# Performance work log

Measured on AMD Instinct MI355X. Metric: run time of the kernel, lower is better.

The kernel has to match this reference:

```python
import jax, jax.numpy as jnp
import numpy as np

N = 30000; E = 480000; B = 60
IN = 200; ID = 128; H = 128
NEXP = 4; TOPK = 2; TEMP = 1.5
HEADS = 4; DH = H // HEADS


def _ln(x, g, b):
    mu = jnp.mean(x, -1, keepdims=True)
    var = jnp.var(x, -1, keepdims=True)
    return (x - mu) / jnp.sqrt(var + 1e-5) * g + b


def _seg_sum(d, i, n):
    return jax.ops.segment_sum(d, i, num_segments=n)


def setup_inputs():
    key = jax.random.key(0)
    kit = iter(jax.random.split(key, 80))
    def w(*s):
        return jax.random.normal(next(kit), s, jnp.float32) * 0.05
    inp = {}
    inp['x'] = jax.random.normal(next(kit), (N, IN), jnp.float32)
    inp['node_identity'] = jax.random.normal(next(kit), (N, ID), jnp.float32)
    inp['edge_index'] = jax.random.randint(next(kit), (2, E), 0, N)
    inp['batch'] = jnp.sort(jax.random.randint(next(kit), (N,), 0, B))
    inp.update(fe_W=w(IN, H), fe_b=jnp.zeros(H), fe_g=jnp.ones(H), fe_be=jnp.zeros(H))
    inp.update(ie_W=w(ID, H), ie_b=jnp.zeros(H), ie_g=jnp.ones(H), ie_be=jnp.zeros(H))
    inp.update(fuse_W=w(2 * H, H), fuse_b=jnp.zeros(H), fuse_g=jnp.ones(H), fuse_be=jnp.zeros(H))
    inp.update(router_W=w(2 * H, NEXP))
    inp.update(mlp_W1=w(H, H), mlp_b1=jnp.zeros(H), mlp_W2=w(H, H), mlp_b2=jnp.zeros(H))
    inp.update(cheb_W=w(2, 2, H, H), cheb_b=jnp.zeros((2, H)))
    inp.update(gt_Wq=w(2, H, H), gt_bq=jnp.zeros((2, H)), gt_Wk=w(2, H, H), gt_bk=jnp.zeros((2, H)),
               gt_Wv=w(2, H, H), gt_bv=jnp.zeros((2, H)), gt_Ws=w(2, H, H), gt_bs=jnp.zeros((2, H)))
    inp.update(gcn_W=w(2, H, H), gcn_b=jnp.zeros((2, H)))
    inp.update(pn_g=jnp.ones((NEXP, H)), pn_b=jnp.zeros((NEXP, H)), expert_scales=jnp.ones(NEXP))
    inp.update(h1_W=w(H, H), h1_b=jnp.zeros(H), h1_g=jnp.ones(H), h1_be=jnp.zeros(H))
    inp.update(h2_W=w(H, H // 2), h2_b=jnp.zeros(H // 2), h2_g=jnp.ones(H // 2), h2_be=jnp.zeros(H // 2))
    inp.update(h3_W=w(H // 2, 2), h3_b=jnp.zeros(2), logit_bias=jnp.zeros(2))
    return inp


def _forward(x, node_identity, edge_index, batch, fe_W, fe_b, fe_g, fe_be, ie_W, ie_b, ie_g, ie_be,
             fuse_W, fuse_b, fuse_g, fuse_be, router_W, mlp_W1, mlp_b1, mlp_W2, mlp_b2, cheb_W, cheb_b,
             gt_Wq, gt_bq, gt_Wk, gt_bk, gt_Wv, gt_bv, gt_Ws, gt_bs, gcn_W, gcn_b, pn_g, pn_b,
             expert_scales, h1_W, h1_b, h1_g, h1_be, h2_W, h2_b, h2_g, h2_be, h3_W, h3_b, logit_bias):
    relu = jax.nn.relu
    src, dst = edge_index[0], edge_index[1]
    # encoders + fuse
    h_x = relu(_ln(x @ fe_W + fe_b, fe_g, fe_be))
    h_id = relu(_ln(node_identity @ ie_W + ie_b, ie_g, ie_be))
    h_router = jnp.concatenate([h_x, h_id], -1)
    h = relu(_ln(h_router @ fuse_W + fuse_b, fuse_g, fuse_be))
    # noisy top-k router (eval: no noise, no dropout)
    node_logits = h_router @ router_W
    probs = jax.nn.softmax(node_logits / TEMP, -1)
    vals, idx = jax.lax.top_k(probs, TOPK)
    wts = vals / jnp.clip(jnp.sum(vals, -1, keepdims=True), 1e-9)
    gates = jnp.zeros_like(probs).at[jnp.arange(N)[:, None], idx].set(wts)  # [N, 4]
    # degree / normalization terms
    ones_e = jnp.ones(E, jnp.float32)
    deg = _seg_sum(ones_e, dst, N)
    dinv = jnp.where(deg > 0, jax.lax.rsqrt(jnp.maximum(deg, 1.0)), 0.0)
    dinvl = jax.lax.rsqrt(deg + 1.0)  # with self loops (GCN)
    enorm = dinv[src] * dinv[dst]
    enorml = dinvl[src] * dinvl[dst]
    def aprop(xx, en, di_self=None):
        out = _seg_sum(xx[src] * en[:, None], dst, N)
        if di_self is not None:
            out = out + xx * di_self[:, None]
        return out
    # Expert 0: MLP (2 layers)
    e0 = relu(h @ mlp_W1 + mlp_b1) @ mlp_W2 + mlp_b2
    # Expert 1: ChebNet K=2 (lambda_max=2 -> L_hat = -A_norm), 2 layers
    z = h
    for l in range(2):
        tx1 = -aprop(z, enorm)
        z = z @ cheb_W[l, 0] + tx1 @ cheb_W[l, 1] + cheb_b[l]
        if l == 0:
            z = relu(z)
    e1 = z
    # Expert 2: Graph Transformer, 2 layers, heads=4, root-weight skip
    z = h
    for l in range(2):
        q = (z @ gt_Wq[l] + gt_bq[l]).reshape(N, HEADS, DH)
        k = (z @ gt_Wk[l] + gt_bk[l]).reshape(N, HEADS, DH)
        v = (z @ gt_Wv[l] + gt_bv[l]).reshape(N, HEADS, DH)
        logits = jnp.sum(q[dst] * k[src], -1) * (1.0 / DH ** 0.5)  # [E, heads]
        m = jax.ops.segment_max(logits, dst, num_segments=N)
        m = jnp.where(jnp.isfinite(m), m, 0.0)
        p = jnp.exp(logits - m[dst])
        denom = jnp.clip(_seg_sum(p, dst, N), 1e-9)
        attn = p / denom[dst]
        agg = _seg_sum(attn[:, :, None] * v[src], dst, N).reshape(N, H)
        z = agg + z @ gt_Ws[l] + gt_bs[l]
        if l == 0:
            z = relu(z)
    e2 = z
    # Expert 3: GCN, 2 layers, self loops
    z = h
    for l in range(2):
        zw = z @ gcn_W[l]
        z = aprop(zw, enorml, dinvl * dinvl) + gcn_b[l]
        if l == 0:
            z = relu(z)
    e3 = z
    # per-expert post-norm, scale, gated combine + residual
    eo = jnp.stack([e0, e1, e2, e3], 0)  # [4, N, H]
    eo = _ln(eo, pn_g[:, None, :], pn_b[:, None, :]) * expert_scales[:, None, None]
    out = h + jnp.einsum('ne,enh->nh', gates, eo)
    # mean-pool readout per graph
    counts = jnp.clip(_seg_sum(jnp.ones(N, jnp.float32), batch, B), 1.0)
    pooled = _seg_sum(out, batch, B) / counts[:, None]
    # classification head
    zc = relu(_ln(pooled @ h1_W + h1_b, h1_g, h1_be))
    zc = relu(_ln(zc @ h2_W + h2_b, h2_g, h2_be))
    return zc @ h3_W + h3_b + logit_bias


def reference(x, node_identity, edge_index, batch, fe_W, fe_b, fe_g, fe_be, ie_W, ie_b, ie_g, ie_be,
              fuse_W, fuse_b, fuse_g, fuse_be, router_W, mlp_W1, mlp_b1, mlp_W2, mlp_b2, cheb_W, cheb_b,
              gt_Wq, gt_bq, gt_Wk, gt_bk, gt_Wv, gt_bv, gt_Ws, gt_bs, gcn_W, gcn_b, pn_g, pn_b,
              expert_scales, h1_W, h1_b, h1_g, h1_be, h2_W, h2_b, h2_g, h2_be, h3_W, h3_b, logit_bias):
    return _forward(x, node_identity, edge_index, batch, fe_W, fe_b, fe_g, fe_be, ie_W, ie_b, ie_g, ie_be,
                    fuse_W, fuse_b, fuse_g, fuse_be, router_W, mlp_W1, mlp_b1, mlp_W2, mlp_b2, cheb_W, cheb_b,
                    gt_Wq, gt_bq, gt_Wk, gt_bk, gt_Wv, gt_bv, gt_Ws, gt_bs, gcn_W, gcn_b, pn_g, pn_b,
                    expert_scales, h1_W, h1_b, h1_g, h1_be, h2_W, h2_b, h2_g, h2_be, h3_W, h3_b, logit_bias)
```

## Files before the change

### kernel.cpp

```cpp
#include <hip/hip_runtime.h>

#define PCH   32
#define NWT   19
#define SCH   2048

typedef unsigned short ushort_t;
typedef __attribute__((ext_vector_type(8))) short bf16x8;
typedef __attribute__((ext_vector_type(4))) float f32x4;

__device__ __forceinline__ float bf2f(unsigned int v) {
    return __uint_as_float(v << 16);
}
__device__ __forceinline__ unsigned int f2bu(float f) {
    unsigned int u = __float_as_uint(f);
    return (u + 0x7fffu + ((u >> 16) & 1u)) >> 16;
}
__device__ __forceinline__ void unpack8(uint4 u, float* f) {
    f[0] = bf2f(u.x & 0xffff); f[1] = bf2f(u.x >> 16);
    f[2] = bf2f(u.y & 0xffff); f[3] = bf2f(u.y >> 16);
    f[4] = bf2f(u.z & 0xffff); f[5] = bf2f(u.z >> 16);
    f[6] = bf2f(u.w & 0xffff); f[7] = bf2f(u.w >> 16);
}
__device__ __forceinline__ uint4 pack8(const float* f) {
    uint4 p;
// ... 182 lines not shown
    const int row_base = m0 + 16 * wv + q * 4;
#pragma unroll
    for (int t = 0; t < 8; t++) {
        float bb = c.bias[t * 16 + l16];
#pragma unroll
        for (int r = 0; r < 4; r++) acc[t][r] += bb;
    }
    float mean[4], inv[4];
#pragma unroll
    for (int r = 0; r < 4; r++) {
        float s = 0.f, sq = 0.f;
#pragma unroll
        for (int t = 0; t < 8; t++) { float v = acc[t][r]; s += v; sq = fmaf(v, v, sq); }
#pragma unroll
        for (int off = 1; off <= 8; off <<= 1) { s += __shfl_xor(s, off); sq += __shfl_xor(sq, off); }
        mean[r] = s * (1.f / 128.f);
        float var = sq * (1.f / 128.f) - mean[r] * mean[r];
        inv[r] = rsqrtf(var + 1e-5f);
    }
    float rl0[4] = {0, 0, 0, 0}, rl1[4] = {0, 0, 0, 0};
    float rl2[4] = {0, 0, 0, 0}, rl3[4] = {0, 0, 0, 0};
#pragma unroll
    for (int t = 0; t < 8; t++) {
        int col = t * 16 + l16;
        float gg = c.g[col], b2 = c.be[col];
        float4 rw = *(const float4*)(c.rW + col * 4);
#pragma unroll
        for (int r = 0; r < 4; r++) {
            float y = fmaxf(fmaf((acc[t][r] - mean[r]) * inv[r], gg, b2), 0.f);
            rl0[r] = fmaf(y, rw.x, rl0[r]);
            rl1[r] = fmaf(y, rw.y, rl1[r]);
            rl2[r] = fmaf(y, rw.z, rl2[r]);
            rl3[r] = fmaf(y, rw.w, rl3[r]);
            float other = __shfl_xor(y, 1);
            int row = row_base + r;
            if (!(l16 & 1) && row < M) {
                unsigned int pk = f2bu(y) | (f2bu(other) << 16);
                *(unsigned int*)(c.Cb + (size_t)row * 256 + col) = pk;
            }
        }
    }
#pragma unroll
    for (int r = 0; r < 4; r++) {
#pragma unroll
        for (int off = 1; off <= 8; off <<= 1) {
            rl0[r] += __shfl_xor(rl0[r], off);
            rl1[r] += __shfl_xor(rl1[r], off);
            rl2[r] += __shfl_xor(rl2[r], off);
            rl3[r] += __shfl_xor(rl3[r], off);
        }
        int row = row_base + r;
        if (l16 == 0 && row < M)
            *(float4*)(c.logits + (size_t)row * 4) = make_float4(rl0[r], rl1[r], rl2[r], rl3[r]);
    }
}

__global__ __launch_bounds__(256)
void scan3_enc_kernel(int* __restrict__ rowptr, const int* __restrict__ bsum,
                      const int* __restrict__ degi,
                      float* __restrict__ dinv, float* __restrict__ dinvl, int N,
                      EncCfg c0, EncCfg c1)
{
    __shared__ ushort_t As[64][40];
    __shared__ ushort_t Bs[128][40];
    int bx = blockIdx.x;
    int ns3 = (N + 255) >> 8;
    int gG = (N + 63) >> 6;
    if (bx < ns3) {
        int i = bx * 256 + threadIdx.x;
        if (i == 0) rowptr[0] = 0;
        if (i < N) {
            rowptr[i + 1] += bsum[i / SCH];
            float deg = (float)degi[i];
            dinv[i] = (deg > 0.f) ? rsqrtf(fmaxf(deg, 1.f)) : 0.f;
            dinvl[i] = rsqrtf(deg + 1.f);
        }
        return;
    }
    int b2 = bx - ns3;
    if (b2 < gG) gemm_f32_ln_dev(As, Bs, c0, b2, N);
    else gemm_f32_ln_dev(As, Bs, c1, b2 - gG, N);
}

__global__ void csr_topk_kernel(const int* __restrict__ src, const int* __restrict__ dst,
                                const int* __restrict__ rowptr, int* __restrict__ cursor,
                                int* __restrict__ csr,
                                const float* __restrict__ dinv, const float* __restrict__ dinvl,
                                float* __restrict__ ecA, float* __restrict__ ecB, int E,
                                const float* __restrict__ la, const float* __restrict__ lb,
                                float* __restrict__ gates, int N)
{
    int bx = blockIdx.x;
    int nc = (E + 255) >> 8;
    if (bx < nc) {
        int e = bx * 256 + threadIdx.x;
        if (e >= E) return;
        int d = dst[e];
        int s = src[e];
        int pos = atomicAdd(&cursor[d], 1);
        int o = rowptr[d] + pos;
        csr[o] = s;
        ecA[o] = dinv[d] * dinv[s];
        ecB[o] = dinvl[d] * dinvl[s];
        return;
    }
    int n = (bx - nc) * 256 + threadIdx.x;
    if (n >= N) return;
    float4 a = *(const float4*)(la + (size_t)n * 4);
    float4 b = *(const float4*)(lb + (size_t)n * 4);
    float l[4] = {(a.x + b.x) * (1.f / 1.5f), (a.y + b.y) * (1.f / 1.5f),
                  (a.z + b.z) * (1.f / 1.5f), (a.w + b.w) * (1.f / 1.5f)};
    float mx = fmaxf(fmaxf(l[0], l[1]), fmaxf(l[2], l[3]));
    float e4[4], ssum = 0.f;
#pragma unroll
    for (int i = 0; i < 4; i++) { e4[i] = expf(l[i] - mx); ssum += e4[i]; }
    float p[4];
#pragma unroll
    for (int i = 0; i < 4; i++) p[i] = e4[i] / ssum;
    int i0 = 0;
    for (int i = 1; i < 4; i++) if (p[i] > p[i0]) i0 = i;
    int i1 = -1;
    for (int i = 0; i < 4; i++) {
        if (i == i0) continue;
        if (i1 < 0 || p[i] > p[i1]) i1 = i;
    }
    float wsum = fmaxf(p[i0] + p[i1], 1e-9f);
    float gg[4] = {0.f, 0.f, 0.f, 0.f};
    gg[i0] = p[i0] / wsum;
    gg[i1] = p[i1] / wsum;
    *(float4*)(gates + (size_t)n * 4) = make_float4(gg[0], gg[1], gg[2], gg[3]);
}

__global__ __launch_bounds__(256)
void gemm_ln256_kernel(const ushort_t* __restrict__ A,
                       const ushort_t* __restrict__ Wt,
                       ushort_t* __restrict__ Cb, int M,
                       const float* __restrict__ bias,
                       const float* __restrict__ g, const float* __restrict__ be)
{
    const int K = 256;
    __shared__ ushort_t As[64][40];
    __shared__ ushort_t Bs[128][40];
    const int tid = threadIdx.x;
    const int m0 = blockIdx.x * 64;
    const int lane = tid & 63;
    const int wv = tid >> 6;
    const int q = lane >> 4;
    const int l16 = lane & 15;
    const int sar = tid >> 2;
    const int sak = (tid & 3) << 3;
    const int sbn = tid >> 1;
    const int sbk = (tid & 1) << 4;
    const bool arow_ok = (m0 + sar) < M;
    const ushort_t* Arow = A + (size_t)(m0 + sar) * K;
    const ushort_t* Wrow = Wt + (size_t)sbn * K;

    f32x4 acc[8];
#pragma unroll
    for (int t = 0; t < 8; t++) acc[t] = (f32x4){0.f, 0.f, 0.f, 0.f};

#pragma unroll
    for (int k0 = 0; k0 < K; k0 += 32) {
        uint4 apk = arow_ok ? *(const uint4*)(Arow + k0 + sak) : make_uint4(0, 0, 0, 0);
        uint4 b0 = *(const uint4*)(Wrow + k0 + sbk);
        uint4 b1 = *(const uint4*)(Wrow + k0 + sbk + 8);
        __syncthreads();
        *(uint4*)&As[sar][sak] = apk;
        *(uint4*)&Bs[sbn][sbk] = b0;
        *(uint4*)&Bs[sbn][sbk + 8] = b1;
        __syncthreads();
        bf16x8 af = *(const bf16x8*)&As[16 * wv + l16][q * 8];
#pragma unroll
        for (int t = 0; t < 8; t++) {
            bf16x8 bf = *(const bf16x8*)&Bs[t * 16 + l16][q * 8];
            acc[t] = __builtin_amdgcn_mfma_f32_16x16x32_bf16(af, bf, acc[t], 0, 0, 0);
        }
    }
    const int row_base = m0 + 16 * wv + q * 4;
#pragma unroll
    for (int t = 0; t < 8; t++) {
        float bb = bias[t * 16 + l16];
#pragma unroll
        for (int r = 0; r < 4; r++) acc[t][r] += bb;
    }
    float mean[4], inv[4];
#pragma unroll
    for (int r = 0; r < 4; r++) {
        float s = 0.f, sq = 0.f;
#pragma unroll
        for (int t = 0; t < 8; t++) { float v = acc[t][r]; s += v; sq = fmaf(v, v, sq); }
#pragma unroll
        for (int off = 1; off <= 8; off <<= 1) { s += __shfl_xor(s, off); sq += __shfl_xor(sq, off); }
        mean[r] = s * (1.f / 128.f);
        float var = sq * (1.f / 128.f) - mean[r] * mean[r];
        inv[r] = rsqrtf(var + 1e-5f);
    }
#pragma unroll
    for (int t = 0; t < 8; t++) {
        int col = t * 16 + l16;
        float gg = g[col], b2 = be[col];
#pragma unroll
        for (int r = 0; r < 4; r++) {
            float y = fmaxf(fmaf((acc[t][r] - mean[r]) * inv[r], gg, b2), 0.f);
            float other = __shfl_xor(y, 1);
            int row = row_base + r;
            if (!(l16 & 1) && row < M) {
                unsigned int pk = f2bu(y) | (f2bu(other) << 16);
                *(unsigned int*)(Cb + (size_t)row * 128 + col) = pk;
            }
        }
    }
}

template <int K>
__device__ __forceinline__ void gemm_bf_dev(ushort_t (*As)[40], ushort_t (*Bs)[40],
                                            const ushort_t* __restrict__ A,
                                            const ushort_t* __restrict__ Wt,
                                            ushort_t* __restrict__ Cb, int M,
                                            const float* __restrict__ bias, int relu, int bx)
{
    const int tid = threadIdx.x;
    const int m0 = bx * 64;
    const int lane = tid & 63;
    const int wv = tid >> 6;
    const int q = lane >> 4;
    const int l16 = lane & 15;
    const int sar = tid >> 2;
    const int sak = (tid & 3) << 3;
    const int sbn = tid >> 1;
    const int sbk = (tid & 1) << 4;
    const bool arow_ok = (m0 + sar) < M;
    const ushort_t* Arow = A + (size_t)(m0 + sar) * K;
    const ushort_t* Wrow = Wt + (size_t)sbn * K;

    f32x4 acc[8];
#pragma unroll
    for (int t = 0; t < 8; t++) acc[t] = (f32x4){0.f, 0.f, 0.f, 0.f};

#pragma unroll
    for (int k0 = 0; k0 < K; k0 += 32) {
        uint4 apk = arow_ok ? *(const uint4*)(Arow + k0 + sak) : make_uint4(0, 0, 0, 0);
        uint4 b0 = *(const uint4*)(Wrow + k0 + sbk);
        uint4 b1 = *(const uint4*)(Wrow + k0 + sbk + 8);
        __syncthreads();
        *(uint4*)&As[sar][sak] = apk;
        *(uint4*)&Bs[sbn][sbk] = b0;
        *(uint4*)&Bs[sbn][sbk + 8] = b1;
        __syncthreads();
        bf16x8 af = *(const bf16x8*)&As[16 * wv + l16][q * 8];
#pragma unroll
        for (int t = 0; t < 8; t++) {
            bf16x8 bf = *(const bf16x8*)&Bs[t * 16 + l16][q * 8];
            acc[t] = __builtin_amdgcn_mfma_f32_16x16x32_bf16(af, bf, acc[t], 0, 0, 0);
        }
    }
#pragma unroll
    for (int t = 0; t < 8; t++) {
        int col = t * 16 + l16;
        float bb = bias ? bias[col] : 0.f;
#pragma unroll
        for (int r = 0; r < 4; r++) {
            int row = m0 + 16 * wv + q * 4 + r;
            float val = acc[t][r] + bb;
            if (relu) val = fmaxf(val, 0.f);
            float other = __shfl_xor(val, 1);
            if (!(lane & 1) && row < M) {
                unsigned int pk = f2bu(val) | (f2bu(other) << 16);
                *(unsigned int*)(Cb + (size_t)row * 128 + col) = pk;
            }
        }
    }
}

__device__ __forceinline__ void gemm_dual_dev(ushort_t (*As)[40], ushort_t (*Bs)[40],
                                              const ushort_t* __restrict__ A1,
                                              const ushort_t* __restrict__ Wt1,
                                              const ushort_t* __restrict__ A2,
                                              const ushort_t* __restrict__ Wt2,
                                              ushort_t* __restrict__ Cb, int M,
                                              const float* __restrict__ bias, int relu, int bx)
{
    const int K = 128;
    const int tid = threadIdx.x;
    const int m0 = bx * 64;
    const int lane = tid & 63;
    const int wv = tid >> 6;
    const int q = lane >> 4;
    const int l16 = lane & 15;
    const int sar = tid >> 2;
    const int sak = (tid & 3) << 3;
    const int sbn = tid >> 1;
    const int sbk = (tid & 1) << 4;
    const bool arow_ok = (m0 + sar) < M;

    f32x4 acc[8];
#pragma unroll
    for (int t = 0; t < 8; t++) acc[t] = (f32x4){0.f, 0.f, 0.f, 0.f};

    for (int ph = 0; ph < 2; ph++) {
        const ushort_t* Arow = (ph ? A2 : A1) + (size_t)(m0 + sar) * K;
        const ushort_t* Wrow = (ph ? Wt2 : Wt1) + (size_t)sbn * K;
        for (int k0 = 0; k0 < K; k0 += 32) {
            uint4 apk = arow_ok ? *(const uint4*)(Arow + k0 + sak) : make_uint4(0, 0, 0, 0);
            uint4 b0 = *(const uint4*)(Wrow + k0 + sbk);
            uint4 b1 = *(const uint4*)(Wrow + k0 + sbk + 8);
            __syncthreads();
            *(uint4*)&As[sar][sak] = apk;
            *(uint4*)&Bs[sbn][sbk] = b0;
            *(uint4*)&Bs[sbn][sbk + 8] = b1;
            __syncthreads();
            bf16x8 af = *(const bf16x8*)&As[16 * wv + l16][q * 8];
#pragma unroll
            for (int t = 0; t < 8; t++) {
                bf16x8 bf = *(const bf16x8*)&Bs[t * 16 + l16][q * 8];
                acc[t] = __builtin_amdgcn_mfma_f32_16x16x32_bf16(af, bf, acc[t], 0, 0, 0);
            }
        }
    }
#pragma unroll
    for (int t = 0; t < 8; t++) {
        int col = t * 16 + l16;
        float bb = bias ? bias[col] : 0.f;
#pragma unroll
        for (int r = 0; r < 4; r++) {
            int row = m0 + 16 * wv + q * 4 + r;
            float val = acc[t][r] + bb;
            if (relu) val = fmaxf(val, 0.f);
            float other = __shfl_xor(val, 1);
            if (!(lane & 1) && row < M) {
                unsigned int pk = f2bu(val) | (f2bu(other) << 16);
                *(unsigned int*)(Cb + (size_t)row * 128 + col) = pk;
            }
        }
    }
}

__device__ __forceinline__ void gemm4_dev(ushort_t (*As)[40], ushort_t (*Bs)[40],
                                          const ushort_t* __restrict__ A,
                                          const ushort_t* __restrict__ Wt,
                                          ushort_t* __restrict__ qb, ushort_t* __restrict__ kv,
                                          ushort_t* __restrict__ sk, int M,
                                          const float* __restrict__ b0, const float* __restrict__ b1,
                                          const float* __restrict__ b2, const float* __restrict__ b3,
                                          int bx)
{
    const int K = 128;
    const int tid = threadIdx.x;
    const int m0 = bx * 64;
    const int lane = tid & 63;
    const int wv = tid >> 6;
    const int q = lane >> 4;
    const int l16 = lane & 15;
    const int sar = tid >> 2;
    const int sak = (tid & 3) << 3;
    const bool arow_ok = (m0 + sar) < M;
    const ushort_t* Arow = A + (size_t)(m0 + sar) * K;

    f32x4 acc[32];
#pragma unroll
    for (int t = 0; t < 32; t++) acc[t] = (f32x4){0.f, 0.f, 0.f, 0.f};

    for (int k0 = 0; k0 < K; k0 += 32) {
        uint4 apk = arow_ok ? *(const uint4*)(Arow + k0 + sak) : make_uint4(0, 0, 0, 0);
        uint4 bv[4][2];
        int rows[4], kofs[4];
#pragma unroll
        for (int j = 0; j < 4; j++) {
            int slot = tid + j * 256;
            rows[j] = slot >> 1;
            kofs[j] = (slot & 1) << 4;
            const ushort_t* Wrow = Wt + (size_t)rows[j] * K + k0 + kofs[j];
            bv[j][0] = *(const uint4*)Wrow;
            bv[j][1] = *(const uint4*)(Wrow + 8);
        }
        __syncthreads();
        *(uint4*)&As[sar][sak] = apk;
#pragma unroll
        for (int j = 0; j < 4; j++) {
            *(uint4*)&Bs[rows[j]][kofs[j]] = bv[j][0];
            *(uint4*)&Bs[rows[j]][kofs[j] + 8] = bv[j][1];
        }
        __syncthreads();
        bf16x8 af = *(const bf16x8*)&As[16 * wv + l16][q * 8];
#pragma unroll
        for (int t = 0; t < 32; t++) {
            bf16x8 bf = *(const bf16x8*)&Bs[t * 16 + l16][q * 8];
            acc[t] = __builtin_amdgcn_mfma_f32_16x16x32_bf16(af, bf, acc[t], 0, 0, 0);
        }
    }
    const float* bs4[4] = {b0, b1, b2, b3};
#pragma unroll
    for (int s = 0; s < 4; s++) {
#pragma unroll
        for (int t8 = 0; t8 < 8; t8++) {
            int t = s * 8 + t8;
            int col = t8 * 16 + l16;
            float bb = bs4[s][col];
#pragma unroll
            for (int r = 0; r < 4; r++) {
                int row = m0 + 16 * wv + q * 4 + r;
                float val = acc[t][r] + bb;
                float other = __shfl_xor(val, 1);
                if (!(lane & 1) && row < M) {
                    unsigned int pk = f2bu(val) | (f2bu(other) << 16);
                    if (s == 0)
                        *(unsigned int*)(qb + (size_t)row * 128 + col) = pk;
                    else if (s == 3)
                        *(unsigned int*)(sk + (size_t)row * 128 + col) = pk;
                    else
                        *(unsigned int*)(kv + (size_t)row * 256 + (s - 1) * 128 + col) = pk;
                }
            }
        }
    }
}

__device__ __forceinline__ void gemm_wv_dev(const ushort_t* __restrict__ A,
                                            const ushort_t* __restrict__ Wt,
                                            ushort_t* __restrict__ Cb, int M,
                                            const float* __restrict__ bias, int relu,
                                            int w, int lane)
{
    const int K = 128;
    int ct = w & 3;
    int rt = w >> 2;
    int row0 = rt * 16;
    if (row0 >= M) return;
    int l16 = lane & 15, q = lane >> 4;
    int arow = row0 + l16;
    bool aok = arow < M;
    const ushort_t* Ar = A + (size_t)arow * K + q * 8;
    const ushort_t* W0 = Wt + (size_t)(ct * 32 + l16) * K + q * 8;
    const ushort_t* W1 = W0 + (size_t)16 * K;
    bf16x8 zz = {0, 0, 0, 0, 0, 0, 0, 0};
    f32x4 a0 = {0.f, 0.f, 0.f, 0.f}, a1 = {0.f, 0.f, 0.f, 0.f};
#pragma unroll
    for (int k0 = 0; k0 < K; k0 += 32) {
        bf16x8 af = aok ? *(const bf16x8*)(Ar + k0) : zz;
        bf16x8 b0 = *(const bf16x8*)(W0 + k0);
        bf16x8 b1 = *(const bf16x8*)(W1 + k0);
        a0 = __builtin_amdgcn_mfma_f32_16x16x32_bf16(af, b0, a0, 0, 0, 0);
        a1 = __builtin_amdgcn_mfma_f32_16x16x32_bf16(af, b1, a1, 0, 0, 0);
    }
    f32x4 av[2] = {a0, a1};
#pragma unroll
    for (int t = 0; t < 2; t++) {
        int col = ct * 32 + t * 16 + l16;
        float bb = bias ? bias[col] : 0.f;
#pragma unroll
        for (int r = 0; r < 4; r++) {
            int row = row0 + q * 4 + r;
            float val = av[t][r] + bb;
            if (relu) val = fmaxf(val, 0.f);
            float other = __shfl_xor(val, 1);
            if (!(l16 & 1) && row < M) {
                unsigned int pk = f2bu(val) | (f2bu(other) << 16);
                *(unsigned int*)(Cb + (size_t)row * 128 + col) = pk;
            }
        }
    }
}

__device__ __forceinline__ void gather2_dev(const ushort_t* __restrict__ Xb,
                                            ushort_t* __restrict__ OutA, ushort_t* __restrict__ OutB,
                                            const int* __restrict__ rowptr, const int* __restrict__ csr,
                                            const float* __restrict__ ecA, const float* __restrict__ ecB,
                                            const float* __restrict__ dinvl, int M, int bx)
{
    int node = bx * 4 + (threadIdx.x >> 6);
// ... 112 lines not shown
    int beg = rowptr[node], end = rowptr[node + 1];
    int slot = lane >> 4, g = lane & 15;
    uint4 qv = *(const uint4*)(Qb + (size_t)node * 128 + g * 8);
    float qf[8];
    unpack8(qv, qf);
#pragma unroll
    for (int j = 0; j < 8; j++) qf[j] *= SCL;
    float ax[8] = {0, 0, 0, 0, 0, 0, 0, 0};
    float den = 0.f;
    for (int e = beg; e < end; e += 8) {
        int r0 = e + slot, r1 = e + 4 + slot;
        bool v0 = r0 < end, v1 = r1 < end;
        int s0 = 0, s1 = 0;
        if (v0) s0 = csr[r0];
        if (v1) s1 = csr[r1];
        const ushort_t* p0 = KV + (size_t)s0 * 256 + g * 8;
        const ushort_t* p1 = KV + (size_t)s1 * 256 + g * 8;
        uint4 k0 = *(const uint4*)p0;
        uint4 k1 = *(const uint4*)p1;
        uint4 u0 = *(const uint4*)(p0 + 128);
        uint4 u1 = *(const uint4*)(p1 + 128);
        float d0 = dot8(k0, qf);
        float d1 = dot8(k1, qf);
        d0 += __shfl_xor(d0, 1); d0 += __shfl_xor(d0, 2);
        d1 += __shfl_xor(d1, 1); d1 += __shfl_xor(d1, 2);
        float w0 = v0 ? exp2f(fminf(d0, 80.f)) : 0.f;
        float w1 = v1 ? exp2f(fminf(d1, 80.f)) : 0.f;
        den += w0 + w1;
        fma8(u0, w0, ax);
        fma8(u1, w1, ax);
    }
#pragma unroll
    for (int j = 0; j < 8; j++) {
        ax[j] += __shfl_xor(ax[j], 16); ax[j] += __shfl_xor(ax[j], 32);
    }
    den += __shfl_xor(den, 16); den += __shfl_xor(den, 32);
    float dd = fmaxf(den, 1e-9f);
    if (lane < 16) {
        uint4 sv = *(const uint4*)(sk + (size_t)node * 128 + g * 8);
        float sf[8];
        unpack8(sv, sf);
        float o[8];
#pragma unroll
        for (int j = 0; j < 8; j++) {
            float v = ax[j] / dd + sf[j];
            o[j] = relu ? fmaxf(v, 0.f) : v;
        }
        *(uint4*)(Outb + (size_t)node * 128 + g * 8) = pack8(o);
    }
}

__global__ void flatA_kernel(const ushort_t* __restrict__ hb,
                             ushort_t* __restrict__ x1, ushort_t* __restrict__ x2,
                             const int* __restrict__ rowptr, const int* __restrict__ csr,
                             const float* __restrict__ ecA, const float* __restrict__ ecB,
                             const float* __restrict__ dinvl, int N,
                             const ushort_t* __restrict__ wmlp1, ushort_t* __restrict__ xm,
                             const float* __restrict__ b18)
{
    int bx = blockIdx.x;
    int gN4 = (N + 3) >> 2;
    if (bx < gN4) {
        gather2_dev(hb, x1, x2, rowptr, csr, ecA, ecB, dinvl, N, bx);
    } else {
        int w = (bx - gN4) * 4 + (threadIdx.x >> 6);
        gemm_wv_dev(hb, wmlp1, xm, N, b18, 1, w, threadIdx.x & 63);
    }
}

__global__ __launch_bounds__(256)
void megaA_kernel(const ushort_t* __restrict__ hb,
                  const ushort_t* __restrict__ wqkvs,
                  ushort_t* __restrict__ qb, ushort_t* __restrict__ kvb, ushort_t* __restrict__ skb,
                  const float* __restrict__ bq, const float* __restrict__ bk,
                  const float* __restrict__ bv, const float* __restrict__ bs,
                  const ushort_t* __restrict__ x1, const ushort_t* __restrict__ wch0,
                  const ushort_t* __restrict__ wch1, ushort_t* __restrict__ x0,
                  const float* __restrict__ bch,
                  const ushort_t* __restrict__ x2, const ushort_t* __restrict__ wgcn,
                  ushort_t* __restrict__ xg1, const float* __restrict__ bgcn,
                  int M)
{
    __shared__ ushort_t As[64][40];
    __shared__ ushort_t Bs[512][40];
    int y = blockIdx.y, bx = blockIdx.x;
    if (y == 0) gemm4_dev(As, Bs, hb, wqkvs, qb, kvb, skb, M, bq, bk, bv, bs, bx);
    else if (y == 1) gemm_dual_dev(As, Bs, hb, wch0, x1, wch1, x0, M, bch, 1, bx);
    else gemm_bf_dev<128>(As, Bs, x2, wgcn, xg1, M, bgcn, 1, bx);
}

__global__ void flatB_kernel(const ushort_t* __restrict__ qb, const ushort_t* __restrict__ kvb,
                             const int* __restrict__ rowptr, const int* __restrict__ csr,
                             const ushort_t* __restrict__ skb, ushort_t* __restrict__ aout,
                             const ushort_t* __restrict__ x0, const ushort_t* __restrict__ xg1,
                             ushort_t* __restrict__ x3, ushort_t* __restrict__ x2,
                             const float* __restrict__ ecA, const float* __restrict__ ecB,
                             const float* __restrict__ dinvl, int N)
{
    int bx = blockIdx.x;
    int gN4 = (N + 3) >> 2;
    if (bx < gN4) gt_attn_dev(qb, kvb, rowptr, csr, skb, 1, aout, N, bx);
    else gather_l2_dev(x0, xg1, x3, x2, rowptr, csr, ecA, ecB, dinvl, N, bx - gN4);
}

__global__ __launch_bounds__(256)
void megaB_kernel(const ushort_t* __restrict__ x1,
                  const ushort_t* __restrict__ wqkvs,
                  ushort_t* __restrict__ qb, ushort_t* __restrict__ kvb, ushort_t* __restrict__ skb,
                  const float* __restrict__ bq, const float* __restrict__ bk,
                  const float* __restrict__ bv, const float* __restrict__ bs,
                  const ushort_t* __restrict__ x0, const ushort_t* __restrict__ wch0,
                  const ushort_t* __restrict__ x3, const ushort_t* __restrict__ wch1,
                  ushort_t* __restrict__ e1b, const float* __restrict__ bch,
                  const ushort_t* __restrict__ x2, const ushort_t* __restrict__ wgcn,
                  ushort_t* __restrict__ e3b, const float* __restrict__ bgcn,
                  const ushort_t* __restrict__ xm, const ushort_t* __restrict__ wmlp2,
                  ushort_t* __restrict__ e0b, const float* __restrict__ bmlp2,
                  int M)
{
    __shared__ ushort_t As[64][40];
    __shared__ ushort_t Bs[512][40];
    int y = blockIdx.y, bx = blockIdx.x;
    if (y == 0) gemm4_dev(As, Bs, x1, wqkvs, qb, kvb, skb, M, bq, bk, bv, bs, bx);
    else if (y == 1) gemm_dual_dev(As, Bs, x0, wch0, x3, wch1, e1b, M, bch, 0, bx);
    else if (y == 2) gemm_bf_dev<128>(As, Bs, x2, wgcn, e3b, M, bgcn, 0, bx);
    else gemm_bf_dev<128>(As, Bs, xm, wmlp2, e0b, M, bmlp2, 0, bx);
}

__global__ void gt_attn2_kernel(const ushort_t* __restrict__ Qb, const ushort_t* __restrict__ KV,
                                const int* __restrict__ rowptr, const int* __restrict__ csr,
                                const ushort_t* __restrict__ sk,
                                ushort_t* __restrict__ Outb, int M)
{
    gt_attn_dev(Qb, KV, rowptr, csr, sk, 0, Outb, M, blockIdx.x);
}

__global__ void pool_combine_kernel(const ushort_t* __restrict__ hb,
                                    const ushort_t* __restrict__ e0, const ushort_t* __restrict__ e1,
                                    const ushort_t* __restrict__ e2, const ushort_t* __restrict__ e3,
                                    const float* __restrict__ gates,
                                    const float* __restrict__ png, const float* __restrict__ pnb,
                                    const float* __restrict__ esc,
                                    const int* __restrict__ bstart, const int* __restrict__ bend,
                                    float* __restrict__ partial)
{
    int b = blockIdx.x, c = blockIdx.y;
    int lane = threadIdx.x;
    int s0 = bstart[b], e0i = bend[b];
    const ushort_t* eps[4] = {e0, e1, e2, e3};
    float ga[4], gb[4], ba[4], bb[4], es[4];
#pragma unroll
    for (int ee = 0; ee < 4; ee++) {
        ga[ee] = png[ee * 128 + lane * 2];
        gb[ee] = png[ee * 128 + lane * 2 + 1];
        ba[ee] = pnb[ee * 128 + lane * 2];
        bb[ee] = pnb[ee * 128 + lane * 2 + 1];
        es[ee] = esc[ee];
    }
    float sx = 0.f, sy = 0.f;
    for (int n = s0 + c; n < e0i; n += PCH) {
        size_t ofs = (size_t)n * 128 + lane * 2;
        float4 gg = *(const float4*)(gates + (size_t)n * 4);
        float gv[4] = {gg.x, gg.y, gg.z, gg.w};
        unsigned int hu = *(const unsigned int*)(hb + ofs);
        float ox = bf2f(hu & 0xffff), oy = bf2f(hu >> 16);
#pragma unroll
        for (int ee = 0; ee < 4; ee++) {
            unsigned int u = *(const unsigned int*)(eps[ee] + ofs);
            float vx = bf2f(u & 0xffff), vy = bf2f(u >> 16);
            float su = vx + vy, sq = vx * vx + vy * vy;
#pragma unroll
            for (int off = 32; off; off >>= 1) { su += __shfl_xor(su, off); sq += __shfl_xor(sq, off); }
            float mean = su * (1.f / 128.f);
            float var = sq * (1.f / 128.f) - mean * mean;
            float inv = rsqrtf(var + 1e-5f);
            float cc = es[ee] * gv[ee];
            ox = fmaf(cc, (vx - mean) * inv * ga[ee] + ba[ee], ox);
            oy = fmaf(cc, (vy - mean) * inv * gb[ee] + bb[ee], oy);
        }
        sx += ox; sy += oy;
    }
    *(float2*)(partial + ((size_t)b * PCH + c) * 128 + lane * 2) = make_float2(sx, sy);
}

__global__ void head_kernel(const float* __restrict__ partial,
                            const int* __restrict__ bstart, const int* __restrict__ bend,
                            const float* __restrict__ h1W, const float* __restrict__ h1b,
                            const float* __restrict__ h1g, const float* __restrict__ h1be,
                            const float* __restrict__ h2W, const float* __restrict__ h2b,
                            const float* __restrict__ h2g, const float* __restrict__ h2be,
                            const float* __restrict__ h3W, const float* __restrict__ h3b,
                            const float* __restrict__ lbias,
                            float* __restrict__ out, int B)
{
    __shared__ float p[128], z[128];
    int b = blockIdx.x, t = threadIdx.x;
    float sum = 0.f;
#pragma unroll
    for (int c = 0; c < PCH; c++) sum += partial[((size_t)b * PCH + c) * 128 + t];
    float cnt = fmaxf((float)(bend[b] - bstart[b]), 1.f);
    p[t] = sum / cnt;
    __syncthreads();
    float a = h1b[t];
    for (int k = 0; k < 128; k++) a = fmaf(p[k], h1W[k * 128 + t], a);
// ... 39 lines not shown

    const int* ei = (const int*)d_in[2];
    const int* src = ei;
    const int* dst = ei + E;
    const int* batch = (const int*)d_in[3];

    const float* W[47];
    for (int i = 0; i < 47; i++) W[i] = (const float*)d_in[i];

    size_t fN = (size_t)N;
    float* gates   = (float*)d_ws;
    float* dinv    = gates + 4 * fN;
    float* dinvl   = dinv + fN;
    float* partial = dinvl + fN;
    float* logitsA = partial + (size_t)128 * B * PCH;
    float* logitsB = logitsA + 4 * fN;
    ushort_t* hb  = (ushort_t*)(logitsB + 4 * fN);
    ushort_t* e0b = hb + 128 * fN;
    ushort_t* e1b = e0b + 128 * fN;
    ushort_t* e2b = e1b + 128 * fN;
    ushort_t* e3b = e2b + 128 * fN;
    ushort_t* x0  = e3b + 128 * fN;
    ushort_t* x1  = x0 + 128 * fN;
    ushort_t* x2  = x1 + 128 * fN;
    ushort_t* x3  = x2 + 128 * fN;
    ushort_t* xm  = x3 + 128 * fN;
    ushort_t* xg1 = xm + 128 * fN;
    ushort_t* skb = xg1 + 128 * fN;
    ushort_t* qb  = skb + 128 * fN;
    ushort_t* kvb = qb + 128 * fN;
    ushort_t* hrb = kvb + 256 * fN;
    ushort_t* wt  = hrb + 256 * fN;
    WtPack wp;
    const float* wsrc[NWT] = {
        W[4], W[8], W[12], W[17], W[19],
        W[21], W[21] + 16384, W[21] + 32768, W[21] + 49152,
        W[23], W[25], W[27], W[29],
        W[23] + 16384, W[25] + 16384, W[27] + 16384, W[29] + 16384,
        W[31], W[31] + 16384
    };
    const int wk[NWT] = {200, 128, 256, 128, 128,
                         128, 128, 128, 128,
                         128, 128, 128, 128,
                         128, 128, 128, 128,
                         128, 128};
    unsigned long long woff[NWT];
    unsigned long long acc_off = 0;
    for (int i = 0; i < NWT; i++) {
        wp.src[i] = wsrc[i];
        wp.K[i] = wk[i];
        wp.off[i] = acc_off;
        woff[i] = acc_off;
        acc_off += (unsigned long long)128 * wk[i];
    }
    int* degi   = (int*)(wt + acc_off + 8);
    int* cursor = degi + N;
    int* rowptr = cursor + N;
    int* csr    = rowptr + (N + 1);
    int* bstart = csr + E;
    int* bend   = bstart + B;
    int* bsum   = bend + B;
    float* ecA  = (float*)(bsum + 256);
    float* ecB  = ecA + E;

    dim3 blk(256);
    int gN4 = (N + 3) / 4;
    int gG = (N + 63) / 64;
    int RT = (N + 15) / 16;
    int nsb = (N + SCH - 1) / SCH;
    int nseg = (N + 255) / 256;
    int nedge = (E + 255) / 256;

    hipMemsetAsync(degi, 0, (size_t)2 * N * sizeof(int), stream);
    hipMemsetAsync(bstart, 0, (size_t)2 * B * sizeof(int), stream);

    setup_mega_kernel<<<dim3(608 + nseg + nedge), blk, 0, stream>>>(
        wp, wt, batch, bstart, bend, N, dst, degi, E);
    scan1_kernel<<<dim3(nsb), blk, 0, stream>>>(degi, rowptr, bsum, N);
    scan2_kernel<<<1, blk, 0, stream>>>(bsum, nsb);
    EncCfg c0 = {W[0], 200, 200, wt + woff[0], hrb, W[5], W[6], W[7], W[16], logitsA};
    EncCfg c1 = {W[1], 128, 128, wt + woff[1], hrb + 128, W[9], W[10], W[11], W[16] + 512, logitsB};
    scan3_enc_kernel<<<dim3(nseg + 2 * gG), blk, 0, stream>>>(
        rowptr, bsum, degi, dinv, dinvl, N, c0, c1);
    csr_topk_kernel<<<dim3(nedge + nseg), blk, 0, stream>>>(
        src, dst, rowptr, cursor, csr, dinv, dinvl, ecA, ecB, E,
        logitsA, logitsB, gates, N);
    gemm_ln256_kernel<<<dim3(gG), blk, 0, stream>>>(hrb, wt + woff[2], hb, N,
                                                    W[13], W[14], W[15]);
    flatA_kernel<<<dim3(gN4 + RT), blk, 0, stream>>>(hb, x1, x2, rowptr, csr, ecA, ecB,
                                                     dinvl, N, wt + woff[3], xm, W[18]);
    megaA_kernel<<<dim3(gG, 3), blk, 0, stream>>>(
        hb, wt + woff[9], qb, kvb, skb, W[24], W[26], W[28], W[30],
        x1, wt + woff[5], wt + woff[6], x0, W[22],
        x2, wt + woff[17], xg1, W[32], N);
    flatB_kernel<<<dim3(2 * gN4), blk, 0, stream>>>(
        qb, kvb, rowptr, csr, skb, x1,
        x0, xg1, x3, x2, ecA, ecB, dinvl, N);
    megaB_kernel<<<dim3(gG, 4), blk, 0, stream>>>(
        x1, wt + woff[13], qb, kvb, skb,
        W[24] + 128, W[26] + 128, W[28] + 128, W[30] + 128,
        x0, wt + woff[7], x3, wt + woff[8], e1b, W[22] + 128,
        x2, wt + woff[18], e3b, W[32] + 128,
        xm, wt + woff[4], e0b, W[20], N);
    gt_attn2_kernel<<<dim3(gN4), blk, 0, stream>>>(qb, kvb, rowptr, csr, skb, e2b, N);
    pool_combine_kernel<<<dim3(B, PCH), dim3(64), 0, stream>>>(
        hb, e0b, e1b, e2b, e3b, gates, W[33], W[34], W[35], bstart, bend, partial);
    head_kernel<<<dim3(B), dim3(128), 0, stream>>>(partial, bstart, bend,
        W[36], W[37], W[38], W[39],
        W[40], W[41], W[42], W[43],
        W[44], W[45], W[46],
        (float*)d_out, B);
}
```

Baseline: 554.6 us.

## Fuse fusion-LN GEMM with CSR build and top-k gating; halve gemm4 shared tile

Merges the 256-K fused GEMM+LayerNorm kernel with the CSR scatter and router top-k kernel into one launch. Block index selects the role, so the independent pieces can run concurrently and one launch is saved. Separately, gemm4_dev now stages its 512-column weight tile into a 256-row shared buffer in two halves per K step. This halves the LDS footprint of megaA/megaB, which should allow more resident blocks, at the cost of two extra barriers per iteration.

```diff
diff --git a/kernel.cpp b/kernel.cpp
--- a/kernel.cpp
+++ b/kernel.cpp
@@ -288,143 +288,15 @@
     else gemm_f32_ln_dev(As, Bs, c1, b2 - gG, N);
 }
 
-__global__ void csr_topk_kernel(const int* __restrict__ src, const int* __restrict__ dst,
-                                const int* __restrict__ rowptr, int* __restrict__ cursor,
-                                int* __restrict__ csr,
-                                const float* __restrict__ dinv, const float* __restrict__ dinvl,
-                                float* __restrict__ ecA, float* __restrict__ ecB, int E,
-                                const float* __restrict__ la, const float* __restrict__ lb,
-                                float* __restrict__ gates, int N)
-{
-    int bx = blockIdx.x;
-    int nc = (E + 255) >> 8;
-    if (bx < nc) {
-        int e = bx * 256 + threadIdx.x;
-        if (e >= E) return;
-        int d = dst[e];
-        int s = src[e];
-        int pos = atomicAdd(&cursor[d], 1);
-        int o = rowptr[d] + pos;
-        csr[o] = s;
-        ecA[o] = dinv[d] * dinv[s];
-        ecB[o] = dinvl[d] * dinvl[s];
-        return;
-    }
-    int n = (bx - nc) * 256 + threadIdx.x;
-    if (n >= N) return;
-    float4 a = *(const float4*)(la + (size_t)n * 4);
-    float4 b = *(const float4*)(lb + (size_t)n * 4);
-    float l[4] = {(a.x + b.x) * (1.f / 1.5f), (a.y + b.y) * (1.f / 1.5f),
-                  (a.z + b.z) * (1.f / 1.5f), (a.w + b.w) * (1.f / 1.5f)};
-    float mx = fmaxf(fmaxf(l[0], l[1]), fmaxf(l[2], l[3]));
-    float e4[4], ssum = 0.f;
-#pragma unroll
-    for (int i = 0; i < 4; i++) { e4[i] = expf(l[i] - mx); ssum += e4[i]; }
-    float p[4];
-#pragma unroll
-    for (int i = 0; i < 4; i++) p[i] = e4[i] / ssum;
-    int i0 = 0;
-    for (int i = 1; i < 4; i++) if (p[i] > p[i0]) i0 = i;
-    int i1 = -1;
-    for (int i = 0; i < 4; i++) {
-        if (i == i0) continue;
-        if (i1 < 0 || p[i] > p[i1]) i1 = i;
-    }
-    float wsum = fmaxf(p[i0] + p[i1], 1e-9f);
-    float gg[4] = {0.f, 0.f, 0.f, 0.f};
-    gg[i0] = p[i0] / wsum;
-    gg[i1] = p[i1] / wsum;
-    *(float4*)(gates + (size_t)n * 4) = make_float4(gg[0], gg[1], gg[2], gg[3]);
-}
-
-__global__ __launch_bounds__(256)
-void gemm_ln256_kernel(const ushort_t* __restrict__ A,
-                       const ushort_t* __restrict__ Wt,
-                       ushort_t* __restrict__ Cb, int M,
-                       const float* __restrict__ bias,
-                       const float* __restrict__ g, const float* __restrict__ be)
+__device__ __forceinline__ void gemm_ln256_dev(ushort_t (*As)[40], ushort_t (*Bs)[40],
+                                               const ushort_t* __restrict__ A,
+                                               const ushort_t* __restrict__ Wt,
+                                               ushort_t* __restrict__ Cb, int M,
+                                               const float* __restrict__ bias,
+                                               const float* __restrict__ g,
+                                               const float* __restrict__ be, int bx)
 {
     const int K = 256;
-    __shared__ ushort_t As[64][40];
-    __shared__ ushort_t Bs[128][40];
-    const int tid = threadIdx.x;
-    const int m0 = blockIdx.x * 64;
-    const int lane = tid & 63;
-    const int wv = tid >> 6;
-    const int q = lane >> 4;
-    const int l16 = lane & 15;
-    const int sar = tid >> 2;
-    const int sak = (tid & 3) << 3;
-    const int sbn = tid >> 1;
-    const int sbk = (tid & 1) << 4;
-    const bool arow_ok = (m0 + sar) < M;
-    const ushort_t* Arow = A + (size_t)(m0 + sar) * K;
-    const ushort_t* Wrow = Wt + (size_t)sbn * K;
-
-    f32x4 acc[8];
-#pragma unroll
-    for (int t = 0; t < 8; t++) acc[t] = (f32x4){0.f, 0.f, 0.f, 0.f};
-
-#pragma unroll
-    for (int k0 = 0; k0 < K; k0 += 32) {
-        uint4 apk = arow_ok ? *(const uint4*)(Arow + k0 + sak) : make_uint4(0, 0, 0, 0);
-        uint4 b0 = *(const uint4*)(Wrow + k0 + sbk);
-        uint4 b1 = *(const uint4*)(Wrow + k0 + sbk + 8);
-        __syncthreads();
-        *(uint4*)&As[sar][sak] = apk;
-        *(uint4*)&Bs[sbn][sbk] = b0;
-        *(uint4*)&Bs[sbn][sbk + 8] = b1;
-        __syncthreads();
-        bf16x8 af = *(const bf16x8*)&As[16 * wv + l16][q * 8];
-#pragma unroll
-        for (int t = 0; t < 8; t++) {
-            bf16x8 bf = *(const bf16x8*)&Bs[t * 16 + l16][q * 8];
-            acc[t] = __builtin_amdgcn_mfma_f32_16x16x32_bf16(af, bf, acc[t], 0, 0, 0);
-        }
-    }
-    const int row_base = m0 + 16 * wv + q * 4;
-#pragma unroll
-    for (int t = 0; t < 8; t++) {
-        float bb = bias[t * 16 + l16];
-#pragma unroll
-        for (int r = 0; r < 4; r++) acc[t][r] += bb;
-    }
-    float mean[4], inv[4];
-#pragma unroll
-    for (int r = 0; r < 4; r++) {
-        float s = 0.f, sq = 0.f;
-#pragma unroll
-        for (int t = 0; t < 8; t++) { float v = acc[t][r]; s += v; sq = fmaf(v, v, sq); }
-#pragma unroll
-        for (int off = 1; off <= 8; off <<= 1) { s += __shfl_xor(s, off); sq += __shfl_xor(sq, off); }
-        mean[r] = s * (1.f / 128.f);
-        float var = sq * (1.f / 128.f) - mean[r] * mean[r];
-        inv[r] = rsqrtf(var + 1e-5f);
-    }
-#pragma unroll
-    for (int t = 0; t < 8; t++) {
-        int col = t * 16 + l16;
-        float gg = g[col], b2 = be[col];
-#pragma unroll
-        for (int r = 0; r < 4; r++) {
-            float y = fmaxf(fmaf((acc[t][r] - mean[r]) * inv[r], gg, b2), 0.f);
-            float other = __shfl_xor(y, 1);
-            int row = row_base + r;
-            if (!(l16 & 1) && row < M) {
-                unsigned int pk = f2bu(y) | (f2bu(other) << 16);
-                *(unsigned int*)(Cb + (size_t)row * 128 + col) = pk;
-            }
-        }
-    }
-}
-
-template <int K>
-__device__ __forceinline__ void gemm_bf_dev(ushort_t (*As)[40], ushort_t (*Bs)[40],
-                                            const ushort_t* __restrict__ A,
-                                            const ushort_t* __restrict__ Wt,
-                                            ushort_t* __restrict__ Cb, int M,
-                                            const float* __restrict__ bias, int relu, int bx)
-{
     const int tid = threadIdx.x;
     const int m0 = bx * 64;
     const int lane = tid & 63;
@@ -460,6 +332,145 @@
             acc[t] = __builtin_amdgcn_mfma_f32_16x16x32_bf16(af, bf, acc[t], 0, 0, 0);
         }
     }
+    const int row_base = m0 + 16 * wv + q * 4;
+#pragma unroll
+    for (int t = 0; t < 8; t++) {
+        float bb = bias[t * 16 + l16];
+#pragma unroll
+        for (int r = 0; r < 4; r++) acc[t][r] += bb;
+    }
+    float mean[4], inv[4];
+#pragma unroll
+    for (int r = 0; r < 4; r++) {
+        float s = 0.f, sq = 0.f;
+#pragma unroll
+        for (int t = 0; t < 8; t++) { float v = acc[t][r]; s += v; sq = fmaf(v, v, sq); }
+#pragma unroll
+        for (int off = 1; off <= 8; off <<= 1) { s += __shfl_xor(s, off); sq += __shfl_xor(sq, off); }
+        mean[r] = s * (1.f / 128.f);
+        float var = sq * (1.f / 128.f) - mean[r] * mean[r];
+        inv[r] = rsqrtf(var + 1e-5f);
+    }
+#pragma unroll
+    for (int t = 0; t < 8; t++) {
+        int col = t * 16 + l16;
+        float gg = g[col], b2 = be[col];
+#pragma unroll
+        for (int r = 0; r < 4; r++) {
+            float y = fmaxf(fmaf((acc[t][r] - mean[r]) * inv[r], gg, b2), 0.f);
+            float other = __shfl_xor(y, 1);
+            int row = row_base + r;
+            if (!(l16 & 1) && row < M) {
+                unsigned int pk = f2bu(y) | (f2bu(other) << 16);
+                *(unsigned int*)(Cb + (size_t)row * 128 + col) = pk;
+            }
+        }
+    }
+}
+
+__global__ __launch_bounds__(256)
+void ln_csr_topk_kernel(const ushort_t* __restrict__ A, const ushort_t* __restrict__ Wt,
+                        ushort_t* __restrict__ Cb, int N,
+                        const float* __restrict__ bias,
+                        const float* __restrict__ g, const float* __restrict__ be,
+                        const int* __restrict__ src, const int* __restrict__ dst,
+                        const int* __restrict__ rowptr, int* __restrict__ cursor,
+                        int* __restrict__ csr,
+                        const float* __restrict__ dinv, const float* __restrict__ dinvl,
+                        float* __restrict__ ecA, float* __restrict__ ecB, int E,
+                        const float* __restrict__ la, const float* __restrict__ lb,
+                        float* __restrict__ gates)
+{
+    __shared__ ushort_t As[64][40];
+    __shared__ ushort_t Bs[128][40];
+    int bx = blockIdx.x;
+    int gG = (N + 63) >> 6;
+    int nedge = (E + 255) >> 8;
+    if (bx < gG) {
+        gemm_ln256_dev(As, Bs, A, Wt, Cb, N, bias, g, be, bx);
+        return;
+    }
+    if (bx < gG + nedge) {
+        int e = (bx - gG) * 256 + threadIdx.x;
+        if (e >= E) return;
+        int d = dst[e];
+        int s = src[e];
+        int pos = atomicAdd(&cursor[d], 1);
+        int o = rowptr[d] + pos;
+        csr[o] = s;
+        ecA[o] = dinv[d] * dinv[s];
+        ecB[o] = dinvl[d] * dinvl[s];
+        return;
+    }
+    int n = (bx - gG - nedge) * 256 + threadIdx.x;
+    if (n >= N) return;
+    float4 a = *(const float4*)(la + (size_t)n * 4);
+    float4 b = *(const float4*)(lb + (size_t)n * 4);
+    float l[4] = {(a.x + b.x) * (1.f / 1.5f), (a.y + b.y) * (1.f / 1.5f),
+                  (a.z + b.z) * (1.f / 1.5f), (a.w + b.w) * (1.f / 1.5f)};
+    float mx = fmaxf(fmaxf(l[0], l[1]), fmaxf(l[2], l[3]));
+    float e4[4], ssum = 0.f;
+#pragma unroll
+    for (int i = 0; i < 4; i++) { e4[i] = expf(l[i] - mx); ssum += e4[i]; }
+    float p[4];
+#pragma unroll
+    for (int i = 0; i < 4; i++) p[i] = e4[i] / ssum;
+    int i0 = 0;
+    for (int i = 1; i < 4; i++) if (p[i] > p[i0]) i0 = i;
+    int i1 = -1;
+    for (int i = 0; i < 4; i++) {
+        if (i == i0) continue;
+        if (i1 < 0 || p[i] > p[i1]) i1 = i;
+    }
+    float wsum = fmaxf(p[i0] + p[i1], 1e-9f);
+    float gg[4] = {0.f, 0.f, 0.f, 0.f};
+    gg[i0] = p[i0] / wsum;
+    gg[i1] = p[i1] / wsum;
+    *(float4*)(gates + (size_t)n * 4) = make_float4(gg[0], gg[1], gg[2], gg[3]);
+}
+
+template <int K>
+__device__ __forceinline__ void gemm_bf_dev(ushort_t (*As)[40], ushort_t (*Bs)[40],
+                                            const ushort_t* __restrict__ A,
+                                            const ushort_t* __restrict__ Wt,
+                                            ushort_t* __restrict__ Cb, int M,
+                                            const float* __restrict__ bias, int relu, int bx)
+{
+    const int tid = threadIdx.x;
+    const int m0 = bx * 64;
+    const int lane = tid & 63;
+    const int wv = tid >> 6;
+    const int q = lane >> 4;
+    const int l16 = lane & 15;
+    const int sar = tid >> 2;
+    const int sak = (tid & 3) << 3;
+    const int sbn = tid >> 1;
+    const int sbk = (tid & 1) << 4;
+    const bool arow_ok = (m0 + sar) < M;
+    const ushort_t* Arow = A + (size_t)(m0 + sar) * K;
+    const ushort_t* Wrow = Wt + (size_t)sbn * K;
+
+    f32x4 acc[8];
+#pragma unroll
+    for (int t = 0; t < 8; t++) acc[t] = (f32x4){0.f, 0.f, 0.f, 0.f};
+
+#pragma unroll
+    for (int k0 = 0; k0 < K; k0 += 32) {
+        uint4 apk = arow_ok ? *(const uint4*)(Arow + k0 + sak) : make_uint4(0, 0, 0, 0);
+        uint4 b0 = *(const uint4*)(Wrow + k0 + sbk);
+        uint4 b1 = *(const uint4*)(Wrow + k0 + sbk + 8);
+        __syncthreads();
+        *(uint4*)&As[sar][sak] = apk;
+        *(uint4*)&Bs[sbn][sbk] = b0;
+        *(uint4*)&Bs[sbn][sbk + 8] = b1;
+        __syncthreads();
+        bf16x8 af = *(const bf16x8*)&As[16 * wv + l16][q * 8];
+#pragma unroll
+        for (int t = 0; t < 8; t++) {
+            bf16x8 bf = *(const bf16x8*)&Bs[t * 16 + l16][q * 8];
+            acc[t] = __builtin_amdgcn_mfma_f32_16x16x32_bf16(af, bf, acc[t], 0, 0, 0);
+        }
+    }
 #pragma unroll
     for (int t = 0; t < 8; t++) {
         int col = t * 16 + l16;
@@ -562,35 +573,58 @@
     const bool arow_ok = (m0 + sar) < M;
     const ushort_t* Arow = A + (size_t)(m0 + sar) * K;
 
+    int rows[2], kofs[2];
+#pragma unroll
+    for (int j = 0; j < 2; j++) {
+        int slot = tid + j * 256;
+        rows[j] = slot >> 1;
+        kofs[j] = (slot & 1) << 4;
+    }
+
     f32x4 acc[32];
 #pragma unroll
     for (int t = 0; t < 32; t++) acc[t] = (f32x4){0.f, 0.f, 0.f, 0.f};
 
     for (int k0 = 0; k0 < K; k0 += 32) {
         uint4 apk = arow_ok ? *(const uint4*)(Arow + k0 + sak) : make_uint4(0, 0, 0, 0);
-        uint4 bv[4][2];
-        int rows[4], kofs[4];
-#pragma unroll
-        for (int j = 0; j < 4; j++) {
-            int slot = tid + j * 256;
-            rows[j] = slot >> 1;
-            kofs[j] = (slot & 1) << 4;
+        uint4 bva[2][2];
+#pragma unroll
+        for (int j = 0; j < 2; j++) {
             const ushort_t* Wrow = Wt + (size_t)rows[j] * K + k0 + kofs[j];
-            bv[j][0] = *(const uint4*)Wrow;
-            bv[j][1] = *(const uint4*)(Wrow + 8);
+            bva[j][0] = *(const uint4*)Wrow;
+            bva[j][1] = *(const uint4*)(Wrow + 8);
         }
         __syncthreads();
         *(uint4*)&As[sar][sak] = apk;
 #pragma unroll
-        for (int j = 0; j < 4; j++) {
-            *(uint4*)&Bs[rows[j]][kofs[j]] = bv[j][0];
-            *(uint4*)&Bs[rows[j]][kofs[j] + 8] = bv[j][1];
+        for (int j = 0; j < 2; j++) {
+            *(uint4*)&Bs[rows[j]][kofs[j]] = bva[j][0];
+            *(uint4*)&Bs[rows[j]][kofs[j] + 8] = bva[j][1];
+        }
+        uint4 bvb[2][2];
+#pragma unroll
+        for (int j = 0; j < 2; j++) {
+            const ushort_t* Wrow = Wt + (size_t)(256 + rows[j]) * K + k0 + kofs[j];
+            bvb[j][0] = *(const uint4*)Wrow;
+            bvb[j][1] = *(const uint4*)(Wrow + 8);
         }
         __syncthreads();
         bf16x8 af = *(const bf16x8*)&As[16 * wv + l16][q * 8];
 #pragma unroll
-        for (int t = 0; t < 32; t++) {
+        for (int t = 0; t < 16; t++) {
             bf16x8 bf = *(const bf16x8*)&Bs[t * 16 + l16][q * 8];
+            acc[t] = __builtin_amdgcn_mfma_f32_16x16x32_bf16(af, bf, acc[t], 0, 0, 0);
+        }
+        __syncthreads();
+#pragma unroll
+        for (int j = 0; j < 2; j++) {
+            *(uint4*)&Bs[rows[j]][kofs[j]] = bvb[j][0];
+            *(uint4*)&Bs[rows[j]][kofs[j] + 8] = bvb[j][1];
+        }
+        __syncthreads();
+#pragma unroll
+        for (int t = 16; t < 32; t++) {
+            bf16x8 bf = *(const bf16x8*)&Bs[(t - 16) * 16 + l16][q * 8];
             acc[t] = __builtin_amdgcn_mfma_f32_16x16x32_bf16(af, bf, acc[t], 0, 0, 0);
         }
     }
@@ -869,7 +903,7 @@
                   int M)
 {
     __shared__ ushort_t As[64][40];
-    __shared__ ushort_t Bs[512][40];
+    __shared__ ushort_t Bs[256][40];
     int y = blockIdx.y, bx = blockIdx.x;
     if (y == 0) gemm4_dev(As, Bs, hb, wqkvs, qb, kvb, skb, M, bq, bk, bv, bs, bx);
     else if (y == 1) gemm_dual_dev(As, Bs, hb, wch0, x1, wch1, x0, M, bch, 1, bx);
@@ -906,7 +940,7 @@
                   int M)
 {
     __shared__ ushort_t As[64][40];
-    __shared__ ushort_t Bs[512][40];
+    __shared__ ushort_t Bs[256][40];
     int y = blockIdx.y, bx = blockIdx.x;
     if (y == 0) gemm4_dev(As, Bs, x1, wqkvs, qb, kvb, skb, M, bq, bk, bv, bs, bx);
     else if (y == 1) gemm_dual_dev(As, Bs, x0, wch0, x3, wch1, e1b, M, bch, 0, bx);
@@ -1112,11 +1146,10 @@
     EncCfg c1 = {W[1], 128, 128, wt + woff[1], hrb + 128, W[9], W[10], W[11], W[16] + 512, logitsB};
     scan3_enc_kernel<<<dim3(nseg + 2 * gG), blk, 0, stream>>>(
         rowptr, bsum, degi, dinv, dinvl, N, c0, c1);
-    csr_topk_kernel<<<dim3(nedge + nseg), blk, 0, stream>>>(
+    ln_csr_topk_kernel<<<dim3(gG + nedge + nseg), blk, 0, stream>>>(
+        hrb, wt + woff[2], hb, N, W[13], W[14], W[15],
         src, dst, rowptr, cursor, csr, dinv, dinvl, ecA, ecB, E,
-        logitsA, logitsB, gates, N);
-    gemm_ln256_kernel<<<dim3(gG), blk, 0, stream>>>(hrb, wt + woff[2], hb, N,
-                                                    W[13], W[14], W[15]);
+        logitsA, logitsB, gates);
     flatA_kernel<<<dim3(gN4 + RT), blk, 0, stream>>>(hb, x1, x2, rowptr, csr, ecA, ecB,
                                                      dinvl, N, wt + woff[3], xm, W[18]);
     megaA_kernel<<<dim3(gG, 3), blk, 0, stream>>>(
```

Result: no change. 550.0 us (-0.8%).
